# Kernel optimization log

Measured on AMD Instinct MI355X. Metric: run time of the kernel, lower is better.

Reference implementation:

```python
import jax, jax.numpy as jnp
import numpy as np

EPS = 1e-6
LN_EPS = 1e-5  # torch.nn.LayerNorm default


def setup_inputs() -> dict:
    key = jax.random.key(0)
    k1, k2, k3, k4 = jax.random.split(key, 4)
    B, T, L, S, C = 32, 512, 5, 9, 64
    x = jax.random.normal(k1, (B, T), dtype=jnp.float32)
    ws = jax.random.uniform(k2, (S, C), dtype=jnp.float32, minval=-1.0, maxval=1.0)
    bs = jax.random.uniform(k3, (S, C), dtype=jnp.float32, minval=-1.0, maxval=1.0)
    loc_emb = 0.02 * jax.random.normal(k4, (L, C), dtype=jnp.float32)
    # scales = base_bias**i for i in -(S-1)//2 .. (S+1)//2 - 1  (base_bias=10, S=9 -> 10^-4..10^4)
    scales = jnp.asarray([10.0 ** i for i in range(-(S - 1) // 2, (S + 1) // 2)], dtype=jnp.float32)
    locs = jnp.asarray([-2.0, -1.0, 0.0, 1.0, 2.0], dtype=jnp.float32)
    return {"x": x, "ws": ws, "bs": bs, "loc_emb": loc_emb, "scales": scales, "locs": locs}


def reference(x, ws, bs, loc_emb, scales, locs):
    # x: (B, T); locs: (L,); scales: (S,); ws/bs: (S, C); loc_emb: (L, C)
    loc_dis = x[..., None] - locs                                  # (B, T, L)
    # location weights
    loc_w = 1.0 / (jnp.log(jnp.abs(loc_dis) + 1.0) + EPS)          # (B, T, L)
    loc_w = loc_w / jnp.sum(loc_w, axis=-1, keepdims=True)
    # scale weights
    scale_w = 1.0 / (jnp.abs(jnp.log(jnp.abs(loc_dis)[..., None] / scales + EPS)) + EPS)  # (B, T, L, S)
    scale_w = scale_w / jnp.sum(scale_w, axis=-1, keepdims=True)
    # broadcast encode: (B, T, L, 1, 1) * (S, C) + (S, C) * (S, 1) -> (B, T, L, S, C)
    enc = loc_dis[..., None, None] * ws + bs * scales[:, None]
    # LayerNorm over channel dim, no affine
    mean = jnp.mean(enc, axis=-1, keepdims=True)
    var = jnp.mean(jnp.square(enc - mean), axis=-1, keepdims=True)
    enc = (enc - mean) * jax.lax.rsqrt(var + LN_EPS)
    # weighted sum over scales -> (B, T, L, C)
    enc = jnp.sum(enc * scale_w[..., None], axis=-2)
    enc = enc + loc_emb
    # weighted sum over locations -> (B, T, C)
    enc = jnp.sum(enc * loc_w[..., None], axis=-2)
    return enc


if __name__ == "__main__":
    out = reference(**setup_inputs())
    print(out.shape, out.dtype)
```

## Files before the change

### kernel.cpp

```cpp
#include <hip/hip_runtime.h>
#include <math.h>


#define EPS_W 1e-6f
#define LN_EPS 1e-5f
#define LOG_EPS -13.815511f

constexpr int L = 5;
constexpr int S = 9;
constexpr int C = 64;
constexpr int POS = 64;

__device__ __forceinline__ float fastrcp(float v) { return __builtin_amdgcn_rcpf(v); }

__global__ __launch_bounds__(256, 1) void mbe3_kernel(
    const float* __restrict__ x,
    const float* __restrict__ ws,
    const float* __restrict__ bs,
    const float* __restrict__ loc_emb,
    const float* __restrict__ scales,
    const float* __restrict__ locs,
    float* __restrict__ out,
    int npos)
{
    const int tid = threadIdx.x;
    const int lane = tid & 63;
    const int wid = tid >> 6;

    __shared__ float stats[S][8];
    __shared__ float4 coefLds[POS][6];

    float w[S], k[S], le[L];
#pragma unroll
    for (int s = 0; s < S; ++s) {
        w[s] = ws[s * C + lane];
        k[s] = bs[s * C + lane] * scales[s];
    }
#pragma unroll
    for (int l = 0; l < L; ++l) le[l] = loc_emb[l * C + lane];

    for (int s = wid; s < S; s += 4) {
        float a0 = w[s], a1 = k[s];
        float a2 = w[s] * w[s], a3 = w[s] * k[s], a4 = k[s] * k[s];
#pragma unroll
        for (int off = 32; off; off >>= 1) {
            a0 += __shfl_xor(a0, off);
            a1 += __shfl_xor(a1, off);
            a2 += __shfl_xor(a2, off);
            a3 += __shfl_xor(a3, off);
            a4 += __shfl_xor(a4, off);
        }
        if (lane == 0) {
            float mww = a0 * (1.0f / 64.0f);
            float mkk = a1 * (1.0f / 64.0f);
            stats[s][0] = mww;
            stats[s][1] = mkk;
            stats[s][2] = fmaf(-mww, mww, a2 * (1.0f / 64.0f));
            stats[s][3] = 2.0f * fmaf(-mww, mkk, a3 * (1.0f / 64.0f));
            stats[s][4] = fmaf(-mkk, mkk, a4 * (1.0f / 64.0f));
            stats[s][5] = __logf(scales[s]);
        }
    }
    __syncthreads();

    const int pbase = blockIdx.x * POS;
    if (wid == 0) {
        const int p = pbase + lane;
        if (p < npos) {
            float mw[S], mk[S], vw[S], c2[S], vk[S], lg[S];
#pragma unroll
            for (int s = 0; s < S; ++s) {
                mw[s] = stats[s][0]; mk[s] = stats[s][1]; vw[s] = stats[s][2];
                c2[s] = stats[s][3]; vk[s] = stats[s][4]; lg[s] = stats[s][5];
            }
            const float xv = x[p];

            float d[L], lwv[L], llog[L];
            float lwsum = 0.0f;
#pragma unroll
            for (int l = 0; l < L; ++l) {
                d[l] = xv - locs[l];
                float ad = fabsf(d[l]);
                lwv[l] = fastrcp(__logf(ad + 1.0f) + EPS_W);
                lwsum += lwv[l];
                llog[l] = __logf(ad);
            }
            const float rlw = fastrcp(lwsum);

            float cf[24];
#pragma unroll
            for (int j = 0; j < 24; ++j) cf[j] = 0.0f;

#pragma unroll
            for (int l = 0; l < L; ++l) {
                const float dd = d[l];
                const float d2 = dd * dd;
                const float lwn = lwv[l] * rlw;
                cf[18 + l] = lwn;

                float swv[S];
                float ssum = 0.0f;
#pragma unroll
                for (int s = 0; s < S; ++s) {
                    float u = fmaxf(llog[l] - lg[s], LOG_EPS);
                    swv[s] = fastrcp(fabsf(u) + EPS_W);
                    ssum += swv[s];
                }
                const float rss = fastrcp(ssum) * lwn;

#pragma unroll
                for (int s = 0; s < S; ++s) {
                    float mean = fmaf(dd, mw[s], mk[s]);
                    float var = fmaf(d2, vw[s], fmaf(dd, c2[s], vk[s]));
                    float rstd = rsqrtf(var + LN_EPS);
                    float alpha = swv[s] * rss * rstd;
                    cf[s] = fmaf(alpha, dd, cf[s]);
                    cf[9 + s] += alpha;
                    cf[23] = fmaf(-alpha, mean, cf[23]);
                }
            }

#pragma unroll
            for (int j = 0; j < 6; ++j)
                coefLds[lane][j] = make_float4(cf[4 * j], cf[4 * j + 1],
                                               cf[4 * j + 2], cf[4 * j + 3]);
        }
    }
    __syncthreads();

    const int rbase = wid * 16;
#pragma unroll
    for (int i = 0; i < 16; ++i) {
        const int row = rbase + i;
        const int p = pbase + row;
        if (p >= npos) break;
        float4 q0 = coefLds[row][0];
        float4 q1 = coefLds[row][1];
        float4 q2 = coefLds[row][2];
        float4 q3 = coefLds[row][3];
        float4 q4 = coefLds[row][4];
        float4 q5 = coefLds[row][5];
        float acc = q5.w;
        acc = fmaf(q0.x, w[0], acc); acc = fmaf(q0.y, w[1], acc);
        acc = fmaf(q0.z, w[2], acc); acc = fmaf(q0.w, w[3], acc);
        acc = fmaf(q1.x, w[4], acc); acc = fmaf(q1.y, w[5], acc);
        acc = fmaf(q1.z, w[6], acc); acc = fmaf(q1.w, w[7], acc);
        acc = fmaf(q2.x, w[8], acc);
        acc = fmaf(q2.y, k[0], acc); acc = fmaf(q2.z, k[1], acc);
        acc = fmaf(q2.w, k[2], acc); acc = fmaf(q3.x, k[3], acc);
        acc = fmaf(q3.y, k[4], acc); acc = fmaf(q3.z, k[5], acc);
        acc = fmaf(q3.w, k[6], acc); acc = fmaf(q4.x, k[7], acc);
        acc = fmaf(q4.y, k[8], acc);
        acc = fmaf(q4.z, le[0], acc); acc = fmaf(q4.w, le[1], acc);
        acc = fmaf(q5.x, le[2], acc); acc = fmaf(q5.y, le[3], acc);
        acc = fmaf(q5.z, le[4], acc);
        out[(size_t)p * C + lane] = acc;
    }
}

extern "C" void kernel_launch(void* const* d_in, const int* in_sizes, int n_in,
                              void* d_out, int out_size, void* d_ws, size_t ws_size,
                              hipStream_t stream) {
    const float* x = (const float*)d_in[0];
    const float* ws = (const float*)d_in[1];
    const float* bs = (const float*)d_in[2];
    const float* loc_emb = (const float*)d_in[3];
    const float* scales = (const float*)d_in[4];
    const float* locs = (const float*)d_in[5];
    float* out = (float*)d_out;

    int npos = in_sizes[0];
    int blocks = (npos + POS - 1) / POS;
    mbe3_kernel<<<blocks, 256, 0, stream>>>(x, ws, bs, loc_emb, scales, locs, out, npos);
}
```

Measured before the change: 13.39 us.

## Split per-position coefficient work across all four waves and drop the second barrier

Each block used to have only wave 0 compute the per-position coefficients for all 64 positions, while the other three waves sat at a barrier. Now each wave computes coefficients for its own 16 positions using lanes 0-15, writes them to its private LDS rows and consumes them itself, so the second __syncthreads goes away. The x load is hoisted ahead of the stats reduction, the stats are packed into float4 LDS entries, and the min-blocks launch-bounds hint is removed. In exchange, only 16 of 64 lanes are active during the coefficient phase, and the code relies on in-order LDS access within a wave with no explicit barrier between the writes and the reads.

```diff
diff --git a/kernel.cpp b/kernel.cpp
--- a/kernel.cpp
+++ b/kernel.cpp
@@ -9,11 +9,12 @@
 constexpr int L = 5;
 constexpr int S = 9;
 constexpr int C = 64;
+constexpr int PW = 16;
 constexpr int POS = 64;
 
 __device__ __forceinline__ float fastrcp(float v) { return __builtin_amdgcn_rcpf(v); }
 
-__global__ __launch_bounds__(256, 1) void mbe3_kernel(
+__global__ __launch_bounds__(256) void mbe4_kernel(
     const float* __restrict__ x,
     const float* __restrict__ ws,
     const float* __restrict__ bs,
@@ -27,8 +28,14 @@
     const int lane = tid & 63;
     const int wid = tid >> 6;
 
-    __shared__ float stats[S][8];
+    __shared__ float4 statsLds[S][2];
     __shared__ float4 coefLds[POS][6];
+
+    const int pbase = blockIdx.x * POS + wid * PW;
+
+    float xv = 0.0f;
+    const int myp = pbase + lane;
+    if (lane < PW && myp < npos) xv = x[myp];
 
     float w[S], k[S], le[L];
 #pragma unroll
@@ -53,87 +60,84 @@
         if (lane == 0) {
             float mww = a0 * (1.0f / 64.0f);
             float mkk = a1 * (1.0f / 64.0f);
-            stats[s][0] = mww;
-            stats[s][1] = mkk;
-            stats[s][2] = fmaf(-mww, mww, a2 * (1.0f / 64.0f));
-            stats[s][3] = 2.0f * fmaf(-mww, mkk, a3 * (1.0f / 64.0f));
-            stats[s][4] = fmaf(-mkk, mkk, a4 * (1.0f / 64.0f));
-            stats[s][5] = __logf(scales[s]);
+            statsLds[s][0] = make_float4(
+                mww, mkk,
+                fmaf(-mww, mww, a2 * (1.0f / 64.0f)),
+                2.0f * fmaf(-mww, mkk, a3 * (1.0f / 64.0f)));
+            statsLds[s][1] = make_float4(
+                fmaf(-mkk, mkk, a4 * (1.0f / 64.0f)),
+                __logf(scales[s]), 0.0f, 0.0f);
         }
     }
     __syncthreads();
 
-    const int pbase = blockIdx.x * POS;
-    if (wid == 0) {
-        const int p = pbase + lane;
-        if (p < npos) {
-            float mw[S], mk[S], vw[S], c2[S], vk[S], lg[S];
+    if (lane < PW && myp < npos) {
+        float mw[S], mk[S], vw[S], c2[S], vk[S], lg[S];
+#pragma unroll
+        for (int s = 0; s < S; ++s) {
+            float4 a = statsLds[s][0];
+            float4 b = statsLds[s][1];
+            mw[s] = a.x; mk[s] = a.y; vw[s] = a.z; c2[s] = a.w;
+            vk[s] = b.x; lg[s] = b.y;
+        }
+
+        float d[L], lwv[L], llog[L];
+        float lwsum = 0.0f;
+#pragma unroll
+        for (int l = 0; l < L; ++l) {
+            d[l] = xv - locs[l];
+            float ad = fabsf(d[l]);
+            lwv[l] = fastrcp(__logf(ad + 1.0f) + EPS_W);
+            lwsum += lwv[l];
+            llog[l] = __logf(ad);
+        }
+        const float rlw = fastrcp(lwsum);
+
+        float cf[24];
+#pragma unroll
+        for (int j = 0; j < 24; ++j) cf[j] = 0.0f;
+
+#pragma unroll
+        for (int l = 0; l < L; ++l) {
+            const float dd = d[l];
+            const float d2 = dd * dd;
+            const float lwn = lwv[l] * rlw;
+            cf[18 + l] = lwn;
+
+            float swv[S];
+            float ssum = 0.0f;
 #pragma unroll
             for (int s = 0; s < S; ++s) {
-                mw[s] = stats[s][0]; mk[s] = stats[s][1]; vw[s] = stats[s][2];
-                c2[s] = stats[s][3]; vk[s] = stats[s][4]; lg[s] = stats[s][5];
+                float u = fmaxf(llog[l] - lg[s], LOG_EPS);
+                swv[s] = fastrcp(fabsf(u) + EPS_W);
+                ssum += swv[s];
             }
-            const float xv = x[p];
-
-            float d[L], lwv[L], llog[L];
-            float lwsum = 0.0f;
-#pragma unroll
-            for (int l = 0; l < L; ++l) {
-                d[l] = xv - locs[l];
-                float ad = fabsf(d[l]);
-                lwv[l] = fastrcp(__logf(ad + 1.0f) + EPS_W);
-                lwsum += lwv[l];
-                llog[l] = __logf(ad);
-            }
-            const float rlw = fastrcp(lwsum);
-
-            float cf[24];
-#pragma unroll
-            for (int j = 0; j < 24; ++j) cf[j] = 0.0f;
+            const float rss = fastrcp(ssum) * lwn;
 
 #pragma unroll
-            for (int l = 0; l < L; ++l) {
-                const float dd = d[l];
-                const float d2 = dd * dd;
-                const float lwn = lwv[l] * rlw;
-                cf[18 + l] = lwn;
+            for (int s = 0; s < S; ++s) {
+                float mean = fmaf(dd, mw[s], mk[s]);
+                float var = fmaf(d2, vw[s], fmaf(dd, c2[s], vk[s]));
+                float rstd = rsqrtf(var + LN_EPS);
+                float alpha = swv[s] * rss * rstd;
+                cf[s] = fmaf(alpha, dd, cf[s]);
+                cf[9 + s] += alpha;
+                cf[23] = fmaf(-alpha, mean, cf[23]);
+            }
+        }
 
-                float swv[S];
-                float ssum = 0.0f;
+        const int row = wid * PW + lane;
 #pragma unroll
-                for (int s = 0; s < S; ++s) {
-                    float u = fmaxf(llog[l] - lg[s], LOG_EPS);
-                    swv[s] = fastrcp(fabsf(u) + EPS_W);
-                    ssum += swv[s];
-                }
-                const float rss = fastrcp(ssum) * lwn;
+        for (int j = 0; j < 6; ++j)
+            coefLds[row][j] = make_float4(cf[4 * j], cf[4 * j + 1],
+                                          cf[4 * j + 2], cf[4 * j + 3]);
+    }
 
 #pragma unroll
-                for (int s = 0; s < S; ++s) {
-                    float mean = fmaf(dd, mw[s], mk[s]);
-                    float var = fmaf(d2, vw[s], fmaf(dd, c2[s], vk[s]));
-                    float rstd = rsqrtf(var + LN_EPS);
-                    float alpha = swv[s] * rss * rstd;
-                    cf[s] = fmaf(alpha, dd, cf[s]);
-                    cf[9 + s] += alpha;
-                    cf[23] = fmaf(-alpha, mean, cf[23]);
-                }
-            }
-
-#pragma unroll
-            for (int j = 0; j < 6; ++j)
-                coefLds[lane][j] = make_float4(cf[4 * j], cf[4 * j + 1],
-                                               cf[4 * j + 2], cf[4 * j + 3]);
-        }
-    }
-    __syncthreads();
-
-    const int rbase = wid * 16;
-#pragma unroll
-    for (int i = 0; i < 16; ++i) {
-        const int row = rbase + i;
-        const int p = pbase + row;
+    for (int i = 0; i < PW; ++i) {
+        const int p = pbase + i;
         if (p >= npos) break;
+        const int row = wid * PW + i;
         float4 q0 = coefLds[row][0];
         float4 q1 = coefLds[row][1];
         float4 q2 = coefLds[row][2];
@@ -171,5 +175,5 @@
 
     int npos = in_sizes[0];
     int blocks = (npos + POS - 1) / POS;
-    mbe3_kernel<<<blocks, 256, 0, stream>>>(x, ws, bs, loc_emb, scales, locs, out, npos);
+    mbe4_kernel<<<blocks, 256, 0, stream>>>(x, ws, bs, loc_emb, scales, locs, out, npos);
 }
```

Result: faster. 12.63 us (-5.7%).
